# Performance work log

Measured on AMD Instinct MI355X. Metric: run time of the kernel, lower is better.

Reference implementation:

```python
import jax, jax.numpy as jnp
import numpy as np

P = 8  # patch_shape (8, 8) -> per-window sequence length 64


def _bias_indices():
    # pairs of (i, j) coords inside an 8x8 patch window
    pairs = np.array([[i, j] for i in range(P) for j in range(P)])  # [64, 2]
    rel = pairs[:, None, :] - pairs[None, :, :] + P - 1  # [64, 64, 2] in [0, 14]
    return rel[:, :, 0], rel[:, :, 1]


def _make_mask(Wy, Wx):
    # generate_mask with apply_shift=True, patch_shape=(8,8)
    s = P // 2
    m = np.zeros((Wy, Wx, P, P, P, P), dtype=bool)
    m[-1, :, :s, :, s:, :] = True
    m[-1, :, s:, :, :s, :] = True
    m[:, -1, :, :s, :, s:] = True
    m[:, -1, :, s:, :, :s] = True
    return jnp.asarray(m.reshape(Wy, Wx, P * P, P * P))


def setup_inputs() -> dict:
    key = jax.random.key(0)
    ks = jax.random.split(key, 10)
    B, Wy, Wx, S, E, H, hd = 16, 16, 16, 64, 128, 4, 32
    sc = 0.05
    return {
        "patches": jax.random.normal(ks[0], (B, Wy, Wx, S, E), dtype=jnp.float32),
        "Wq": jax.random.normal(ks[1], (H, E, hd), dtype=jnp.float32) * sc,
        "bq": jax.random.normal(ks[2], (H, hd), dtype=jnp.float32) * sc,
        "Wk": jax.random.normal(ks[3], (H, E, hd), dtype=jnp.float32) * sc,
        "bk": jax.random.normal(ks[4], (H, hd), dtype=jnp.float32) * sc,
        "Wv": jax.random.normal(ks[5], (H, E, hd), dtype=jnp.float32) * sc,
        "bv": jax.random.normal(ks[6], (H, hd), dtype=jnp.float32) * sc,
        "pos_bias": jax.random.normal(ks[7], (2 * P - 1, 2 * P - 1), dtype=jnp.float32) * 0.02,
        "Wo": jax.random.normal(ks[8], (E, E), dtype=jnp.float32) * sc,
        "bo": jax.random.normal(ks[9], (E,), dtype=jnp.float32) * sc,
        "mask": _make_mask(Wy, Wx),
    }


def reference(patches, Wq, bq, Wk, bk, Wv, bv, pos_bias, Wo, bo, mask):
    hd = Wq.shape[-1]
    B, Wy, Wx, S, E = patches.shape
    H = Wq.shape[0]
    # per-head Q/K/V projections (torch loops over heads; here batched over h)
    q = jnp.einsum("bvwse,hed->bvwhsd", patches, Wq) + bq[:, None, :]
    k = jnp.einsum("bvwse,hed->bvwhsd", patches, Wk) + bk[:, None, :]
    v = jnp.einsum("bvwse,hed->bvwhsd", patches, Wv) + bv[:, None, :]
    logits = jnp.einsum("bvwhqd,bvwhkd->bvwhqk", q, k) / jnp.sqrt(jnp.asarray(hd, patches.dtype))
    ri, ci = _bias_indices()
    logits = logits + pos_bias[ri, ci]  # gather [15,15] -> [64,64]
    logits = jnp.where(mask[None, :, :, None, :, :], -jnp.inf, logits)
    attn = jax.nn.softmax(logits, axis=-1)
    out = jnp.einsum("bvwhqk,bvwhkd->bvwhqd", attn, v)
    # concat heads: [..., H, S, hd] -> [..., S, H*hd]
    out = jnp.swapaxes(out, 3, 4).reshape(B, Wy, Wx, S, H * hd)
    return jnp.einsum("bvwse,ef->bvwsf", out, Wo) + bo
```

## Files before the change

kernel.cpp:

```cpp
#include <hip/hip_runtime.h>
#include <hip/hip_bf16.h>

typedef float f32x4 __attribute__((ext_vector_type(4)));
typedef short bf16x8 __attribute__((ext_vector_type(8)));
typedef short s16x4 __attribute__((ext_vector_type(4)));
typedef unsigned int u32;

#define MFMA16(a, b, c) __builtin_amdgcn_mfma_f32_16x16x32_bf16((a), (b), (c), 0, 0, 0)

__device__ __forceinline__ unsigned short f2bf(float x) {
    union { float f; unsigned int u; } a; a.f = x;
    unsigned int r = a.u + 0x7fffu + ((a.u >> 16) & 1u);
    return (unsigned short)(r >> 16);
}

__global__ void prep_kernel(const float* __restrict__ Wq, const float* __restrict__ bq,
                            const float* __restrict__ Wk, const float* __restrict__ bk,
                            const float* __restrict__ Wv, const float* __restrict__ bv,
                            const float* __restrict__ pos_bias, const float* __restrict__ Wo,
                            unsigned short* __restrict__ WT, unsigned short* __restrict__ WoT,
                            float* __restrict__ bqkv, float* __restrict__ bm) {
    const float LOG2E = 1.4426950408889634f;
    int t = blockIdx.x * blockDim.x + threadIdx.x;
    int nt = gridDim.x * blockDim.x;
    for (int i = t; i < 384 * 128; i += nt) {
        int c = i >> 7, kk = i & 127;
        int h = c / 96, rem = c - h * 96, p = rem >> 5, n = rem & 31;
        const float* W = (p == 0) ? Wq : (p == 1 ? Wk : Wv);
        WT[i] = f2bf(W[(h * 128 + kk) * 32 + n]);
    }
    for (int i = t; i < 128 * 128; i += nt) {
        int n = i >> 7, kk = i & 127;
        WoT[i] = f2bf(Wo[kk * 128 + n]);
    }
    for (int i = t; i < 384; i += nt) {
        int h = i / 96, rem = i - h * 96, p = rem >> 5, n = rem & 31;
        const float* b = (p == 0) ? bq : (p == 1 ? bk : bv);
        bqkv[i] = b[h * 32 + n];
    }
    for (int i = t; i < 4 * 4 * 4 * 64 * 4; i += nt) {
        int r = i & 3, l = (i >> 2) & 63, kt = (i >> 8) & 3, qt = (i >> 10) & 3, v = (i >> 12) & 3;
        int q = qt * 16 + (l & 15);
        int k = kt * 16 + ((l >> 4) << 2) + r;
        int qi = q >> 3, qj = q & 7, ki = k >> 3, kj = k & 7;
        bool masked = (((v >> 1) != 0) && ((qi < 4) != (ki < 4))) ||
                      (((v & 1) != 0) && ((qj < 4) != (kj < 4)));
        bm[i] = masked ? -1e30f : pos_bias[(qi - ki + 7) * 15 + (qj - kj + 7)] * LOG2E;
    }
}

__launch_bounds__(256, 3)
__global__ void swin_kernel(const float* __restrict__ patches,
                            const unsigned short* __restrict__ WT,
                            const float* __restrict__ bqkv,
                            const float* __restrict__ bm,
                            const unsigned short* __restrict__ WoT,
                            const float* __restrict__ bo,
                            float* __restrict__ out) {
    __shared__ short lds[24576];
    const int win = blockIdx.x;
    const int wy = (win >> 4) & 15, wx = win & 15;
    const int tid = threadIdx.x;
    const int lane = tid & 63;
    const int h = tid >> 6;
    const int l15 = lane & 15, l4 = lane >> 4;
    const int sw15 = (l15 & 7) << 3;
    const f32x4 zero = {0.f, 0.f, 0.f, 0.f};

    {
        const float4* src = reinterpret_cast<const float4*>(patches + (size_t)win * 8192);
        #pragma unroll
        for (int i = 0; i < 8; ++i) {
            int idx4 = i * 256 + tid;
            float4 v = src[idx4];
            int row = idx4 >> 5;
            int col = (idx4 & 31) << 2;
            s16x4 pk;
            pk[0] = (short)f2bf(v.x); pk[1] = (short)f2bf(v.y);
            pk[2] = (short)f2bf(v.z); pk[3] = (short)f2bf(v.w);
            *reinterpret_cast<s16x4*>(&lds[row * 128 + (col ^ ((row & 7) << 3))]) = pk;
        }
    }
    __syncthreads();

    const int qkbase = 8192 + h * 4096;
    const int vbase = h * 2048;

    bf16x8 xa[4][4];
    #pragma unroll
    for (int mt = 0; mt < 4; ++mt)
        #pragma unroll
        for (int ks = 0; ks < 4; ++ks)
            xa[mt][ks] = *reinterpret_cast<const bf16x8*>(
                &lds[(mt * 16 + l15) * 128 + ((ks * 32 + l4 * 8) ^ sw15)]);

    #pragma unroll
    for (int ct = 0; ct < 4; ++ct) {
        bf16x8 wb[4];
        #pragma unroll
        for (int ks = 0; ks < 4; ++ks)
            wb[ks] = *reinterpret_cast<const bf16x8*>(
                &WT[(h * 96 + ct * 16 + l15) * 128 + ks * 32 + l4 * 8]);
        float b4[4];
        #pragma unroll
        for (int r = 0; r < 4; ++r) b4[r] = bqkv[h * 96 + ct * 16 + l4 * 4 + r];
        #pragma unroll
        for (int mt = 0; mt < 4; ++mt) {
            f32x4 a = zero;
            #pragma unroll
            for (int ks = 0; ks < 4; ++ks) a = MFMA16(wb[ks], xa[mt][ks], a);
            int tok = mt * 16 + l15;
            int cc0 = (ct * 16 + l4 * 4) ^ sw15;
            s16x4 pk;
            #pragma unroll
            for (int r = 0; r < 4; ++r) pk[r] = (short)f2bf(a[r] + b4[r]);
            *reinterpret_cast<s16x4*>(&lds[qkbase + tok * 64 + cc0]) = pk;
        }
    }
    __syncthreads();

    #pragma unroll
    for (int ctv = 0; ctv < 2; ++ctv) {
        bf16x8 wb[4];
        #pragma unroll
        for (int ks = 0; ks < 4; ++ks)
            wb[ks] = *reinterpret_cast<const bf16x8*>(
                &WT[(h * 96 + 64 + ctv * 16 + l15) * 128 + ks * 32 + l4 * 8]);
        float bb = bqkv[h * 96 + 64 + ctv * 16 + l15];
        #pragma unroll
        for (int mt = 0; mt < 4; ++mt) {
            f32x4 a = zero;
            #pragma unroll
            for (int ks = 0; ks < 4; ++ks) a = MFMA16(xa[mt][ks], wb[ks], a);
            int n = ctv * 16 + l15;
            int tok0 = (mt * 16 + l4 * 4) ^ sw15;
            s16x4 pk;
            #pragma unroll
            for (int r = 0; r < 4; ++r) pk[r] = (short)f2bf(a[r] + bb);
            *reinterpret_cast<s16x4*>(&lds[vbase + n * 64 + tok0]) = pk;
        }
    }

    bf16x8 kfrag[4], vf[2][2];
    #pragma unroll
    for (int kt = 0; kt < 4; ++kt)
        kfrag[kt] = *reinterpret_cast<const bf16x8*>(
            &lds[qkbase + (kt * 16 + l15) * 64 + ((32 + l4 * 8) ^ sw15)]);
    #pragma unroll
    for (int nt = 0; nt < 2; ++nt)
        #pragma unroll
        for (int ks = 0; ks < 2; ++ks)
            vf[nt][ks] = *reinterpret_cast<const bf16x8*>(
                &lds[vbase + (nt * 16 + l15) * 64 + ((ks * 32 + l4 * 8) ^ sw15)]);

    f32x4 O[2][4];
    #pragma unroll
    for (int nt = 0; nt < 2; ++nt)
        #pragma unroll
        for (int qt = 0; qt < 4; ++qt) O[nt][qt] = zero;

    const int mv = ((wy == 15) ? 2 : 0) + ((wx == 15) ? 1 : 0);
    const float4* bmv = reinterpret_cast<const float4*>(bm);
    const float rs2 = 0.2550348660629988f;
    const int sA = ((l4 & 1) << 5) + l15;
    const int sB = sA + 16;

    #pragma unroll
    for (int qt = 0; qt < 4; ++qt) {
        bf16x8 qfrag = *reinterpret_cast<const bf16x8*>(
            &lds[qkbase + (qt * 16 + l15) * 64 + ((l4 * 8) ^ sw15)]);
        f32x4 LT[4];
        #pragma unroll
        for (int kt = 0; kt < 4; ++kt) LT[kt] = MFMA16(kfrag[kt], qfrag, zero);

        float x[4][4];
        float m = -3.0e38f;
        #pragma unroll
        for (int kt = 0; kt < 4; ++kt) {
            float4 b4 = bmv[((mv * 4 + qt) * 4 + kt) * 64 + lane];
            x[kt][0] = LT[kt][0] * rs2 + b4.x;
            x[kt][1] = LT[kt][1] * rs2 + b4.y;
            x[kt][2] = LT[kt][2] * rs2 + b4.z;
            x[kt][3] = LT[kt][3] * rs2 + b4.w;
            m = fmaxf(m, fmaxf(fmaxf(x[kt][0], x[kt][1]), fmaxf(x[kt][2], x[kt][3])));
        }
        m = fmaxf(m, __shfl_xor(m, 16));
        m = fmaxf(m, __shfl_xor(m, 32));
        float s = 0.f;
        #pragma unroll
        for (int kt = 0; kt < 4; ++kt)
            #pragma unroll
            for (int r = 0; r < 4; ++r) {
                float e = exp2f(x[kt][r] - m);
                x[kt][r] = e;
                s += e;
            }
        s += __shfl_xor(s, 16);
        s += __shfl_xor(s, 32);
        float inv = 1.0f / s;

        u32 w[4][2];
        #pragma unroll
        for (int kt = 0; kt < 4; ++kt) {
            w[kt][0] = (u32)f2bf(x[kt][0] * inv) | ((u32)f2bf(x[kt][1] * inv) << 16);
            w[kt][1] = (u32)f2bf(x[kt][2] * inv) | ((u32)f2bf(x[kt][3] * inv) << 16);
        }
        u32 fr[2][4];
        #pragma unroll
        for (int kt = 0; kt < 4; ++kt) {
            u32 a0 = __shfl(w[kt][0], sA);
            u32 a1 = __shfl(w[kt][1], sA);
            u32 b0 = __shfl(w[kt][0], sB);
            u32 b1 = __shfl(w[kt][1], sB);
            if ((kt & 1) == (l4 >> 1)) {
                const int ks = kt >> 1;
                fr[ks][0] = a0; fr[ks][1] = a1; fr[ks][2] = b0; fr[ks][3] = b1;
            }
        }
        bf16x8 pf0, pf1;
        {
            union { u32 u[4]; bf16x8 v; } c0, c1;
            c0.u[0] = fr[0][0]; c0.u[1] = fr[0][1]; c0.u[2] = fr[0][2]; c0.u[3] = fr[0][3];
            c1.u[0] = fr[1][0]; c1.u[1] = fr[1][1]; c1.u[2] = fr[1][2]; c1.u[3] = fr[1][3];
            pf0 = c0.v; pf1 = c1.v;
        }
        #pragma unroll
        for (int nt = 0; nt < 2; ++nt) {
            O[nt][qt] = MFMA16(vf[nt][0], pf0, O[nt][qt]);
            O[nt][qt] = MFMA16(vf[nt][1], pf1, O[nt][qt]);
        }
    }
    __syncthreads();

    #pragma unroll
    for (int nt = 0; nt < 2; ++nt)
        #pragma unroll
        for (int qt = 0; qt < 4; ++qt) {
            int q = qt * 16 + l15;
            int f0 = (h * 32 + nt * 16 + l4 * 4) ^ sw15;
            s16x4 pk;
            #pragma unroll
            for (int r = 0; r < 4; ++r) pk[r] = (short)f2bf(O[nt][qt][r]);
            *reinterpret_cast<s16x4*>(&lds[8192 + q * 128 + f0]) = pk;
        }
    __syncthreads();

    {
        bf16x8 wf[2][4];
        #pragma unroll
        for (int nt = 0; nt < 2; ++nt)
            #pragma unroll
            for (int ks = 0; ks < 4; ++ks)
                wf[nt][ks] = *reinterpret_cast<const bf16x8*>(
                    &WoT[(h * 32 + nt * 16 + l15) * 128 + ks * 32 + l4 * 8]);
        float4 bo4[2];
        #pragma unroll
        for (int nt = 0; nt < 2; ++nt)
            bo4[nt] = *reinterpret_cast<const float4*>(&bo[h * 32 + nt * 16 + l4 * 4]);
        float* outw = out + (size_t)win * 8192;
        #pragma unroll
        for (int mt = 0; mt < 4; ++mt) {
            bf16x8 af[4];
            #pragma unroll
            for (int ks = 0; ks < 4; ++ks)
                af[ks] = *reinterpret_cast<const bf16x8*>(
                    &lds[8192 + (mt * 16 + l15) * 128 + ((ks * 32 + l4 * 8) ^ sw15)]);
            #pragma unroll
            for (int nt = 0; nt < 2; ++nt) {
                f32x4 a = zero;
                #pragma unroll
                for (int ks = 0; ks < 4; ++ks) a = MFMA16(wf[nt][ks], af[ks], a);
                float4 st;
                st.x = a[0] + bo4[nt].x;
                st.y = a[1] + bo4[nt].y;
                st.z = a[2] + bo4[nt].z;
                st.w = a[3] + bo4[nt].w;
                *reinterpret_cast<float4*>(
                    &outw[(size_t)(mt * 16 + l15) * 128 + h * 32 + nt * 16 + l4 * 4]) = st;
            }
        }
    }
}

extern "C" void kernel_launch(void* const* d_in, const int* in_sizes, int n_in,
                              void* d_out, int out_size, void* d_ws, size_t ws_size,
                              hipStream_t stream) {
    const float* patches  = (const float*)d_in[0];
    const float* Wq       = (const float*)d_in[1];
    const float* bq       = (const float*)d_in[2];
    const float* Wk       = (const float*)d_in[3];
    const float* bk       = (const float*)d_in[4];
    const float* Wv       = (const float*)d_in[5];
    const float* bv       = (const float*)d_in[6];
    const float* pos_bias = (const float*)d_in[7];
    const float* Wo       = (const float*)d_in[8];
    const float* bo       = (const float*)d_in[9];

    char* ws = (char*)d_ws;
    unsigned short* WT  = (unsigned short*)(ws);
    unsigned short* WoT = (unsigned short*)(ws + 98304);
    float* bqkv         = (float*)(ws + 131072);
    float* bm           = (float*)(ws + 132608);

    hipLaunchKernelGGL(prep_kernel, dim3(64), dim3(256), 0, stream,
                       Wq, bq, Wk, bk, Wv, bv, pos_bias, Wo, WT, WoT, bqkv, bm);
    hipLaunchKernelGGL(swin_kernel, dim3(4096), dim3(256), 0, stream,
                       patches, WT, bqkv, bm, WoT, bo, (float*)d_out);
}
```

Baseline: 110.0 us.

## Keep Q/K in registers via shuffles, shrink LDS, raise occupancy, add setprio

Q and K projection results are redistributed into MFMA fragments through cross-lane shuffles and held in registers, so they never round-trip through LDS. This lets shared memory shrink and the launch bound rise to 4 blocks per CU. The change also uses hardware packed bf16 conversion, prefetches the bias/mask tiles one query tile ahead, hoists the Wo weight loads, and wraps MFMA sections in s_setprio. The costs are more shuffle instructions and higher register pressure under the tighter launch bound, which risks spilling.

```diff
diff --git a/kernel.cpp b/kernel.cpp
--- a/kernel.cpp
+++ b/kernel.cpp
@@ -7,6 +7,12 @@
 typedef unsigned int u32;
 
 #define MFMA16(a, b, c) __builtin_amdgcn_mfma_f32_16x16x32_bf16((a), (b), (c), 0, 0, 0)
+
+__device__ __forceinline__ u32 pk2(float lo, float hi) {
+    union { __hip_bfloat162 h; u32 u; } c;
+    c.h = __float22bfloat162_rn(float2{lo, hi});
+    return c.u;
+}
 
 __device__ __forceinline__ unsigned short f2bf(float x) {
     union { float f; unsigned int u; } a; a.f = x;
@@ -49,7 +55,7 @@
     }
 }
 
-__launch_bounds__(256, 3)
+__launch_bounds__(256, 4)
 __global__ void swin_kernel(const float* __restrict__ patches,
                             const unsigned short* __restrict__ WT,
                             const float* __restrict__ bqkv,
@@ -57,15 +63,18 @@
                             const unsigned short* __restrict__ WoT,
                             const float* __restrict__ bo,
                             float* __restrict__ out) {
-    __shared__ short lds[24576];
+    __shared__ short lds[16384];
     const int win = blockIdx.x;
-    const int wy = (win >> 4) & 15, wx = win & 15;
     const int tid = threadIdx.x;
     const int lane = tid & 63;
     const int h = tid >> 6;
     const int l15 = lane & 15, l4 = lane >> 4;
     const int sw15 = (l15 & 7) << 3;
     const f32x4 zero = {0.f, 0.f, 0.f, 0.f};
+    const int sA = ((l4 & 1) << 5) + l15;
+    const int sB = sA + 16;
+    const float rs2 = 0.2550348660629988f;
+    const float4* bmv = reinterpret_cast<const float4*>(bm);
 
     {
         const float4* src = reinterpret_cast<const float4*>(patches + (size_t)win * 8192);
@@ -73,18 +82,14 @@
         for (int i = 0; i < 8; ++i) {
             int idx4 = i * 256 + tid;
             float4 v = src[idx4];
-            int row = idx4 >> 5;
-            int col = (idx4 & 31) << 2;
-            s16x4 pk;
-            pk[0] = (short)f2bf(v.x); pk[1] = (short)f2bf(v.y);
-            pk[2] = (short)f2bf(v.z); pk[3] = (short)f2bf(v.w);
-            *reinterpret_cast<s16x4*>(&lds[row * 128 + (col ^ ((row & 7) << 3))]) = pk;
+            int row = idx4 >> 5, col = (idx4 & 31) << 2;
+            union { u32 u[2]; s16x4 s; } pk;
+            pk.u[0] = pk2(v.x, v.y);
+            pk.u[1] = pk2(v.z, v.w);
+            *reinterpret_cast<s16x4*>(&lds[row * 128 + (col ^ ((row & 7) << 3))]) = pk.s;
         }
     }
     __syncthreads();
-
-    const int qkbase = 8192 + h * 4096;
-    const int vbase = h * 2048;
 
     bf16x8 xa[4][4];
     #pragma unroll
@@ -93,7 +98,9 @@
         for (int ks = 0; ks < 4; ++ks)
             xa[mt][ks] = *reinterpret_cast<const bf16x8*>(
                 &lds[(mt * 16 + l15) * 128 + ((ks * 32 + l4 * 8) ^ sw15)]);
-
+    __syncthreads();
+
+    bf16x8 qf[4], kf[4];
     #pragma unroll
     for (int ct = 0; ct < 4; ++ct) {
         bf16x8 wb[4];
@@ -107,17 +114,23 @@
         #pragma unroll
         for (int mt = 0; mt < 4; ++mt) {
             f32x4 a = zero;
+            __builtin_amdgcn_s_setprio(1);
             #pragma unroll
             for (int ks = 0; ks < 4; ++ks) a = MFMA16(wb[ks], xa[mt][ks], a);
-            int tok = mt * 16 + l15;
-            int cc0 = (ct * 16 + l4 * 4) ^ sw15;
-            s16x4 pk;
-            #pragma unroll
-            for (int r = 0; r < 4; ++r) pk[r] = (short)f2bf(a[r] + b4[r]);
-            *reinterpret_cast<s16x4*>(&lds[qkbase + tok * 64 + cc0]) = pk;
-        }
-    }
-    __syncthreads();
+            __builtin_amdgcn_s_setprio(0);
+            u32 pw0 = pk2(a[0] + b4[0], a[1] + b4[1]);
+            u32 pw1 = pk2(a[2] + b4[2], a[3] + b4[3]);
+            u32 e0 = __shfl(pw0, sA);
+            u32 e1 = __shfl(pw1, sA);
+            u32 e2 = __shfl(pw0, sB);
+            u32 e3 = __shfl(pw1, sB);
+            if ((ct & 1) == (l4 >> 1)) {
+                union { u32 u[4]; bf16x8 v; } c;
+                c.u[0] = e0; c.u[1] = e1; c.u[2] = e2; c.u[3] = e3;
+                if (ct < 2) qf[mt] = c.v; else kf[mt] = c.v;
+            }
+        }
+    }
 
     #pragma unroll
     for (int ctv = 0; ctv < 2; ++ctv) {
@@ -127,6 +140,7 @@
             wb[ks] = *reinterpret_cast<const bf16x8*>(
                 &WT[(h * 96 + 64 + ctv * 16 + l15) * 128 + ks * 32 + l4 * 8]);
         float bb = bqkv[h * 96 + 64 + ctv * 16 + l15];
+        __builtin_amdgcn_s_setprio(1);
         #pragma unroll
         for (int mt = 0; mt < 4; ++mt) {
             f32x4 a = zero;
@@ -134,24 +148,21 @@
             for (int ks = 0; ks < 4; ++ks) a = MFMA16(xa[mt][ks], wb[ks], a);
             int n = ctv * 16 + l15;
             int tok0 = (mt * 16 + l4 * 4) ^ sw15;
-            s16x4 pk;
-            #pragma unroll
-            for (int r = 0; r < 4; ++r) pk[r] = (short)f2bf(a[r] + bb);
-            *reinterpret_cast<s16x4*>(&lds[vbase + n * 64 + tok0]) = pk;
-        }
-    }
-
-    bf16x8 kfrag[4], vf[2][2];
-    #pragma unroll
-    for (int kt = 0; kt < 4; ++kt)
-        kfrag[kt] = *reinterpret_cast<const bf16x8*>(
-            &lds[qkbase + (kt * 16 + l15) * 64 + ((32 + l4 * 8) ^ sw15)]);
+            union { u32 u[2]; s16x4 s; } pk;
+            pk.u[0] = pk2(a[0] + bb, a[1] + bb);
+            pk.u[1] = pk2(a[2] + bb, a[3] + bb);
+            *reinterpret_cast<s16x4*>(&lds[h * 2048 + n * 64 + tok0]) = pk.s;
+        }
+        __builtin_amdgcn_s_setprio(0);
+    }
+
+    bf16x8 vf[2][2];
     #pragma unroll
     for (int nt = 0; nt < 2; ++nt)
         #pragma unroll
         for (int ks = 0; ks < 2; ++ks)
             vf[nt][ks] = *reinterpret_cast<const bf16x8*>(
-                &lds[vbase + (nt * 16 + l15) * 64 + ((ks * 32 + l4 * 8) ^ sw15)]);
+                &lds[h * 2048 + (nt * 16 + l15) * 64 + ((ks * 32 + l4 * 8) ^ sw15)]);
 
     f32x4 O[2][4];
     #pragma unroll
@@ -159,29 +170,34 @@
         #pragma unroll
         for (int qt = 0; qt < 4; ++qt) O[nt][qt] = zero;
 
-    const int mv = ((wy == 15) ? 2 : 0) + ((wx == 15) ? 1 : 0);
-    const float4* bmv = reinterpret_cast<const float4*>(bm);
-    const float rs2 = 0.2550348660629988f;
-    const int sA = ((l4 & 1) << 5) + l15;
-    const int sB = sA + 16;
+    const int mv = (((win >> 4) & 15) == 15 ? 2 : 0) + ((win & 15) == 15 ? 1 : 0);
+
+    float4 bcur[4], bnxt[4];
+    #pragma unroll
+    for (int kt = 0; kt < 4; ++kt) bcur[kt] = bmv[((mv * 4 + 0) * 4 + kt) * 64 + lane];
 
     #pragma unroll
     for (int qt = 0; qt < 4; ++qt) {
-        bf16x8 qfrag = *reinterpret_cast<const bf16x8*>(
-            &lds[qkbase + (qt * 16 + l15) * 64 + ((l4 * 8) ^ sw15)]);
         f32x4 LT[4];
-        #pragma unroll
-        for (int kt = 0; kt < 4; ++kt) LT[kt] = MFMA16(kfrag[kt], qfrag, zero);
+        __builtin_amdgcn_s_setprio(1);
+        #pragma unroll
+        for (int kt = 0; kt < 4; ++kt) LT[kt] = MFMA16(kf[kt], qf[qt], zero);
+        __builtin_amdgcn_s_setprio(0);
+
+        if (qt < 3) {
+            #pragma unroll
+            for (int kt = 0; kt < 4; ++kt)
+                bnxt[kt] = bmv[((mv * 4 + qt + 1) * 4 + kt) * 64 + lane];
+        }
 
         float x[4][4];
         float m = -3.0e38f;
         #pragma unroll
         for (int kt = 0; kt < 4; ++kt) {
-            float4 b4 = bmv[((mv * 4 + qt) * 4 + kt) * 64 + lane];
-            x[kt][0] = LT[kt][0] * rs2 + b4.x;
-            x[kt][1] = LT[kt][1] * rs2 + b4.y;
-            x[kt][2] = LT[kt][2] * rs2 + b4.z;
-            x[kt][3] = LT[kt][3] * rs2 + b4.w;
+            x[kt][0] = LT[kt][0] * rs2 + bcur[kt].x;
+            x[kt][1] = LT[kt][1] * rs2 + bcur[kt].y;
+            x[kt][2] = LT[kt][2] * rs2 + bcur[kt].z;
+            x[kt][3] = LT[kt][3] * rs2 + bcur[kt].w;
             m = fmaxf(m, fmaxf(fmaxf(x[kt][0], x[kt][1]), fmaxf(x[kt][2], x[kt][3])));
         }
         m = fmaxf(m, __shfl_xor(m, 16));
@@ -199,19 +215,19 @@
         s += __shfl_xor(s, 32);
         float inv = 1.0f / s;
 
-        u32 w[4][2];
+        u32 wp[4][2];
         #pragma unroll
         for (int kt = 0; kt < 4; ++kt) {
-            w[kt][0] = (u32)f2bf(x[kt][0] * inv) | ((u32)f2bf(x[kt][1] * inv) << 16);
-            w[kt][1] = (u32)f2bf(x[kt][2] * inv) | ((u32)f2bf(x[kt][3] * inv) << 16);
+            wp[kt][0] = pk2(x[kt][0] * inv, x[kt][1] * inv);
+            wp[kt][1] = pk2(x[kt][2] * inv, x[kt][3] * inv);
         }
         u32 fr[2][4];
         #pragma unroll
         for (int kt = 0; kt < 4; ++kt) {
-            u32 a0 = __shfl(w[kt][0], sA);
-            u32 a1 = __shfl(w[kt][1], sA);
-            u32 b0 = __shfl(w[kt][0], sB);
-            u32 b1 = __shfl(w[kt][1], sB);
+            u32 a0 = __shfl(wp[kt][0], sA);
+            u32 a1 = __shfl(wp[kt][1], sA);
+            u32 b0 = __shfl(wp[kt][0], sB);
+            u32 b1 = __shfl(wp[kt][1], sB);
             if ((kt & 1) == (l4 >> 1)) {
                 const int ks = kt >> 1;
                 fr[ks][0] = a0; fr[ks][1] = a1; fr[ks][2] = b0; fr[ks][3] = b1;
@@ -224,13 +240,31 @@
             c1.u[0] = fr[1][0]; c1.u[1] = fr[1][1]; c1.u[2] = fr[1][2]; c1.u[3] = fr[1][3];
             pf0 = c0.v; pf1 = c1.v;
         }
+        __builtin_amdgcn_s_setprio(1);
         #pragma unroll
         for (int nt = 0; nt < 2; ++nt) {
             O[nt][qt] = MFMA16(vf[nt][0], pf0, O[nt][qt]);
             O[nt][qt] = MFMA16(vf[nt][1], pf1, O[nt][qt]);
         }
-    }
-    __syncthreads();
+        __builtin_amdgcn_s_setprio(0);
+
+        if (qt < 3) {
+            #pragma unroll
+            for (int kt = 0; kt < 4; ++kt) bcur[kt] = bnxt[kt];
+        }
+    }
+
+    bf16x8 wf[2][4];
+    #pragma unroll
+    for (int nt = 0; nt < 2; ++nt)
+        #pragma unroll
+        for (int ks = 0; ks < 4; ++ks)
+            wf[nt][ks] = *reinterpret_cast<const bf16x8*>(
+                &WoT[(h * 32 + nt * 16 + l15) * 128 + ks * 32 + l4 * 8]);
+    float4 bo4[2];
+    #pragma unroll
+    for (int nt = 0; nt < 2; ++nt)
+        bo4[nt] = *reinterpret_cast<const float4*>(&bo[h * 32 + nt * 16 + l4 * 4]);
 
     #pragma unroll
     for (int nt = 0; nt < 2; ++nt)
@@ -238,25 +272,14 @@
         for (int qt = 0; qt < 4; ++qt) {
             int q = qt * 16 + l15;
             int f0 = (h * 32 + nt * 16 + l4 * 4) ^ sw15;
-            s16x4 pk;
-            #pragma unroll
-            for (int r = 0; r < 4; ++r) pk[r] = (short)f2bf(O[nt][qt][r]);
-            *reinterpret_cast<s16x4*>(&lds[8192 + q * 128 + f0]) = pk;
+            union { u32 u[2]; s16x4 s; } pk;
+            pk.u[0] = pk2(O[nt][qt][0], O[nt][qt][1]);
+            pk.u[1] = pk2(O[nt][qt][2], O[nt][qt][3]);
+            *reinterpret_cast<s16x4*>(&lds[8192 + q * 128 + f0]) = pk.s;
         }
     __syncthreads();
 
     {
-        bf16x8 wf[2][4];
-        #pragma unroll
-        for (int nt = 0; nt < 2; ++nt)
-            #pragma unroll
-            for (int ks = 0; ks < 4; ++ks)
-                wf[nt][ks] = *reinterpret_cast<const bf16x8*>(
-                    &WoT[(h * 32 + nt * 16 + l15) * 128 + ks * 32 + l4 * 8]);
-        float4 bo4[2];
-        #pragma unroll
-        for (int nt = 0; nt < 2; ++nt)
-            bo4[nt] = *reinterpret_cast<const float4*>(&bo[h * 32 + nt * 16 + l4 * 4]);
         float* outw = out + (size_t)win * 8192;
         #pragma unroll
         for (int mt = 0; mt < 4; ++mt) {
@@ -265,6 +288,7 @@
             for (int ks = 0; ks < 4; ++ks)
                 af[ks] = *reinterpret_cast<const bf16x8*>(
                     &lds[8192 + (mt * 16 + l15) * 128 + ((ks * 32 + l4 * 8) ^ sw15)]);
+            __builtin_amdgcn_s_setprio(1);
             #pragma unroll
             for (int nt = 0; nt < 2; ++nt) {
                 f32x4 a = zero;
@@ -278,6 +302,7 @@
                 *reinterpret_cast<float4*>(
                     &outw[(size_t)(mt * 16 + l15) * 128 + h * 32 + nt * 16 + l4 * 4]) = st;
             }
+            __builtin_amdgcn_s_setprio(0);
         }
     }
 }
```

After: 133.4 us. 1.21x slower.
